# Kernel optimization log

Hardware: AMD Instinct MI355X
Metric: run time of the kernel (lower is better)

## Reference

```python
import jax, jax.numpy as jnp
import numpy as np

N_EDGES = 200_000
N_ANGLES = 1_000_000
D = 128          # atom_embed_dim
N_RBF = 6
A_DIM = 49       # n_spher * l_spher
N_BIL = 8        # n_bilinear


def _glorot(key, shape):
    fan_in, fan_out = shape[0], shape[-1]
    lim = jnp.sqrt(6.0 / (fan_in + fan_out))
    return jax.random.uniform(key, shape, jnp.float32, -lim, lim)


def setup_inputs() -> dict:
    key = jax.random.key(0)
    ks = jax.random.split(key, 10)
    m_ji = jax.random.normal(ks[0], (N_EDGES, D), jnp.float32)
    nbr_list = jax.random.randint(ks[1], (N_EDGES, 2), 0, 20000)
    angle_list = jax.random.randint(ks[2], (N_ANGLES, 3), 0, 20000)
    e_rbf = jax.random.normal(ks[3], (N_EDGES, N_RBF), jnp.float32)
    a_sbf = jax.random.normal(ks[4], (N_ANGLES, A_DIM), jnp.float32)
    kj_idx = jax.random.randint(ks[5], (N_ANGLES,), 0, N_EDGES)
    # parameters (torch Linear weight transposed to [in, out])
    W_nbr = _glorot(ks[6], (D, D))
    b_nbr = jnp.zeros((D,), jnp.float32)
    W_e = _glorot(ks[7], (N_RBF, D))
    W_a = _glorot(ks[8], (A_DIM, N_BIL))
    final_w = _glorot(ks[9], (D, N_BIL, D))  # [i, j, l]
    return {
        "m_ji": m_ji, "nbr_list": nbr_list, "angle_list": angle_list,
        "e_rbf": e_rbf, "a_sbf": a_sbf, "kj_idx": kj_idx,
        "W_nbr": W_nbr, "b_nbr": b_nbr, "W_e": W_e, "W_a": W_a,
        "final_w": final_w,
    }


def reference(m_ji, nbr_list, angle_list, e_rbf, a_sbf, kj_idx,
              W_nbr, b_nbr, W_e, W_a, final_w):
    # gather edge messages/radial features per angle (triplet)
    m_kj = m_ji[kj_idx]                                  # [W, D]
    transf_m = jax.nn.silu(m_kj @ W_nbr + b_nbr)         # swish(Linear)
    transf_e = e_rbf[kj_idx] @ W_e                       # [W, D]
    m_and_e = transf_m * transf_e                        # [W, D]
    transf_a = a_sbf @ W_a                               # [W, n_bilinear]
    # bilinear contraction per angle: out[w,i] = sum_{j,l} a[w,j] me[w,l] T[i,j,l]
    out = jnp.einsum('wj,wl,ijl->wi', transf_a, m_and_e, final_w)
    # scatter back to edges (dim_size = n_edges)
    final = jax.ops.segment_sum(out, kj_idx, num_segments=m_ji.shape[0])
    return final
```

## Files before the change

kernel.cpp:

```cpp
#include <hip/hip_runtime.h>
#include <math.h>

#define D 128
#define N_RBF 6
#define A_DIM 49
#define N_BIL 8
#define N_EDGES 200000
#define N_ANGLES 1000000

#define BM 128
#define THREADS 512
#define MROW 132

__device__ __forceinline__ int swz(int row, int col) {
  return (row << 7) + (col ^ (((row >> 3) & 7) << 2));
}

__global__ __launch_bounds__(256) void k_accA(const float* __restrict__ a_sbf,
                                              const int* __restrict__ kj,
                                              const float* __restrict__ W_a,
                                              float* __restrict__ A) {
  __shared__ float wa[A_DIM * N_BIL];
  for (int i = threadIdx.x; i < A_DIM * N_BIL; i += 256) wa[i] = W_a[i];
  __syncthreads();
  int w = blockIdx.x * 256 + threadIdx.x;
  const int stride = gridDim.x * 256;
  for (; w < N_ANGLES; w += stride) {
    const float* ar = a_sbf + (size_t)w * A_DIM;
    float ta[N_BIL];
#pragma unroll
    for (int j = 0; j < N_BIL; ++j) ta[j] = 0.f;
#pragma unroll
    for (int k = 0; k < A_DIM; ++k) {
      const float av = ar[k];
#pragma unroll
      for (int j = 0; j < N_BIL; ++j) ta[j] = fmaf(av, wa[k * N_BIL + j], ta[j]);
    }
    const int e = kj[w];
    float* Ae = A + (size_t)e * N_BIL;
#pragma unroll
    for (int j = 0; j < N_BIL; ++j) atomicAdd(Ae + j, ta[j]);
  }
}

__global__ __launch_bounds__(THREADS, 2) void k_main(const float* __restrict__ m_ji,
                                                     const float* __restrict__ e_rbf,
                                                     const float* __restrict__ W_nbr,
                                                     const float* __restrict__ b_nbr,
                                                     const float* __restrict__ W_e,
                                                     const float* __restrict__ T,
                                                     const float* __restrict__ A,
                                                     float* __restrict__ out) {
  __shared__ float me_lds[BM * MROW];
  __shared__ float tjb[D * D];
  __shared__ float A_lds[BM * N_BIL];
  __shared__ float we_lds[N_RBF * D];
  __shared__ float erbf_lds[BM * N_RBF];

  const int t = threadIdx.x;
  const int e0 = blockIdx.x * BM;
  const int tr = t >> 4;
  const int ti = t & 15;
  const int r0 = tr * 4;
  const int i0 = ti * 8;

  {
    const float4* gm = reinterpret_cast<const float4*>(m_ji);
#pragma unroll
    for (int it = 0; it < 8; ++it) {
      const int q = it * THREADS + t;
      const int r = q >> 5, c4 = q & 31;
      size_t grow = (size_t)(e0 + r);
      if (grow >= N_EDGES) grow = N_EDGES - 1;
      const float4 v = gm[grow * 32 + c4];
      *reinterpret_cast<float4*>(&me_lds[r * MROW + c4 * 4]) = v;
    }
  }
  {
    const float4* gw = reinterpret_cast<const float4*>(W_nbr);
#pragma unroll
    for (int it = 0; it < 8; ++it) {
      const int q = it * THREADS + t;
      const int k = q >> 5, i4 = q & 31;
      const float4 v = gw[k * 32 + i4];
      tjb[swz(i4 * 4 + 0, k)] = v.x;
      tjb[swz(i4 * 4 + 1, k)] = v.y;
      tjb[swz(i4 * 4 + 2, k)] = v.z;
      tjb[swz(i4 * 4 + 3, k)] = v.w;
    }
  }
  for (int q = t; q < BM * N_RBF; q += THREADS) {
    size_t g = (size_t)e0 * N_RBF + q;
    if (g >= (size_t)N_EDGES * N_RBF) g = (size_t)N_EDGES * N_RBF - 1;
    erbf_lds[q] = e_rbf[g];
  }
  for (int q = t; q < N_RBF * D; q += THREADS) we_lds[q] = W_e[q];
  for (int q = t; q < BM * N_BIL; q += THREADS) {
    size_t g = (size_t)e0 * N_BIL + q;
    if (g >= (size_t)N_EDGES * N_BIL) g = (size_t)N_EDGES * N_BIL - 1;
    A_lds[q] = A[g];
  }
  __syncthreads();

  float tm[4][8];
#pragma unroll
  for (int a = 0; a < 4; ++a)
#pragma unroll
    for (int b = 0; b < 8; ++b) tm[a][b] = 0.f;

#pragma unroll 2
  for (int kc = 0; kc < 32; ++kc) {
    float4 mv[4];
#pragma unroll
    for (int rr = 0; rr < 4; ++rr)
      mv[rr] = *reinterpret_cast<const float4*>(&me_lds[(r0 + rr) * MROW + kc * 4]);
    float4 wv[8];
#pragma unroll
    for (int ii = 0; ii < 8; ++ii)
      wv[ii] = *reinterpret_cast<const float4*>(&tjb[swz(i0 + ii, kc * 4)]);
#pragma unroll
    for (int rr = 0; rr < 4; ++rr)
#pragma unroll
      for (int ii = 0; ii < 8; ++ii) {
        tm[rr][ii] = fmaf(mv[rr].x, wv[ii].x, tm[rr][ii]);
        tm[rr][ii] = fmaf(mv[rr].y, wv[ii].y, tm[rr][ii]);
        tm[rr][ii] = fmaf(mv[rr].z, wv[ii].z, tm[rr][ii]);
        tm[rr][ii] = fmaf(mv[rr].w, wv[ii].w, tm[rr][ii]);
      }
  }

  float bi[8];
#pragma unroll
  for (int ii = 0; ii < 8; ++ii) bi[ii] = b_nbr[i0 + ii];
  float me[4][8];
#pragma unroll
  for (int rr = 0; rr < 4; ++rr)
#pragma unroll
    for (int ii = 0; ii < 8; ++ii) {
      const float x = tm[rr][ii] + bi[ii];
      const float s = x / (1.f + expf(-x));
      float te = 0.f;
#pragma unroll
      for (int q = 0; q < N_RBF; ++q)
        te = fmaf(erbf_lds[(r0 + rr) * N_RBF + q], we_lds[q * D + i0 + ii], te);
      me[rr][ii] = s * te;
    }
  __syncthreads();
#pragma unroll
  for (int rr = 0; rr < 4; ++rr)
#pragma unroll
    for (int ii = 0; ii < 8; ++ii) me_lds[(r0 + rr) * MROW + i0 + ii] = me[rr][ii];

  float acc[4][8];
#pragma unroll
  for (int a = 0; a < 4; ++a)
#pragma unroll
    for (int b = 0; b < 8; ++b) acc[a][b] = 0.f;

  for (int j = 0; j < N_BIL; ++j) {
    __syncthreads();
#pragma unroll
    for (int it = 0; it < 8; ++it) {
      const int q = it * THREADS + t;
      const int i = q >> 5, l4 = q & 31;
      const float4 v =
          *reinterpret_cast<const float4*>(&T[((size_t)i * N_BIL + j) * D + l4 * 4]);
      *reinterpret_cast<float4*>(&tjb[swz(i, l4 * 4)]) = v;
    }
    __syncthreads();

    float P[4][8];
#pragma unroll
    for (int a = 0; a < 4; ++a)
#pragma unroll
      for (int b = 0; b < 8; ++b) P[a][b] = 0.f;

#pragma unroll 2
    for (int lc = 0; lc < 32; ++lc) {
      float4 mev[4];
#pragma unroll
      for (int rr = 0; rr < 4; ++rr)
        mev[rr] = *reinterpret_cast<const float4*>(&me_lds[(r0 + rr) * MROW + lc * 4]);
      float4 tv[8];
#pragma unroll
      for (int ii = 0; ii < 8; ++ii)
        tv[ii] = *reinterpret_cast<const float4*>(&tjb[swz(i0 + ii, lc * 4)]);
#pragma unroll
      for (int rr = 0; rr < 4; ++rr)
#pragma unroll
        for (int ii = 0; ii < 8; ++ii) {
          P[rr][ii] = fmaf(mev[rr].x, tv[ii].x, P[rr][ii]);
          P[rr][ii] = fmaf(mev[rr].y, tv[ii].y, P[rr][ii]);
          P[rr][ii] = fmaf(mev[rr].z, tv[ii].z, P[rr][ii]);
          P[rr][ii] = fmaf(mev[rr].w, tv[ii].w, P[rr][ii]);
        }
    }
#pragma unroll
    for (int rr = 0; rr < 4; ++rr) {
      const float aj = A_lds[(r0 + rr) * N_BIL + j];
#pragma unroll
      for (int ii = 0; ii < 8; ++ii) acc[rr][ii] = fmaf(aj, P[rr][ii], acc[rr][ii]);
    }
  }

#pragma unroll
  for (int rr = 0; rr < 4; ++rr) {
    const int erow = e0 + r0 + rr;
    if (erow < N_EDGES) {
      float4 o0 = make_float4(acc[rr][0], acc[rr][1], acc[rr][2], acc[rr][3]);
      float4 o1 = make_float4(acc[rr][4], acc[rr][5], acc[rr][6], acc[rr][7]);
      float* op = out + (size_t)erow * D + i0;
      *reinterpret_cast<float4*>(op) = o0;
      *reinterpret_cast<float4*>(op + 4) = o1;
    }
  }
}

extern "C" void kernel_launch(void* const* d_in, const int* in_sizes, int n_in,
                              void* d_out, int out_size, void* d_ws, size_t ws_size,
                              hipStream_t stream) {
  const float* m_ji  = (const float*)d_in[0];
  const float* e_rbf = (const float*)d_in[3];
  const float* a_sbf = (const float*)d_in[4];
  const int*   kj    = (const int*)d_in[5];
  const float* W_nbr = (const float*)d_in[6];
  const float* b_nbr = (const float*)d_in[7];
  const float* W_e   = (const float*)d_in[8];
  const float* W_a   = (const float*)d_in[9];
  const float* T     = (const float*)d_in[10];

  float* A   = (float*)d_ws;
  float* out = (float*)d_out;

  hipMemsetAsync(A, 0, (size_t)N_EDGES * N_BIL * sizeof(float), stream);
  k_accA<<<(N_ANGLES + 255) / 256, 256, 0, stream>>>(a_sbf, kj, W_a, A);
  k_main<<<(N_EDGES + BM - 1) / BM, THREADS, 0, stream>>>(m_ji, e_rbf, W_nbr, b_nbr, W_e,
                                                          T, A, out);
}
```

Baseline: 1.636 ms.

## Stage a_sbf through LDS, prefetch T slices into registers, simplify swizzle addressing

k_accA now has each block stage its 256×49 slice of a_sbf into shared memory with coalesced float4 loads, replacing strided per-thread row reads, and drops the grid-stride loop. k_main prefetches the next T slice into registers while the current slice is consumed, precomputes the swizzle XOR offset per thread, raises inner-loop unrolling to 8, and removes the min-blocks launch bound. The larger LDS footprint in k_accA and the higher register pressure in k_main may reduce occupancy.

```diff
diff --git a/kernel.cpp b/kernel.cpp
--- a/kernel.cpp
+++ b/kernel.cpp
@@ -20,13 +20,33 @@
                                               const int* __restrict__ kj,
                                               const float* __restrict__ W_a,
                                               float* __restrict__ A) {
+  __shared__ float sa[256 * A_DIM];
   __shared__ float wa[A_DIM * N_BIL];
-  for (int i = threadIdx.x; i < A_DIM * N_BIL; i += 256) wa[i] = W_a[i];
+  const int t = threadIdx.x;
+  const int blk0 = blockIdx.x * 256;
+
+  for (int q = t; q < A_DIM * N_BIL; q += 256) wa[q] = W_a[q];
+  {
+    const size_t fbase = (size_t)blk0 * A_DIM;
+    const float4* g4 = reinterpret_cast<const float4*>(a_sbf + fbase);
+    const int remain4 = (int)(((size_t)N_ANGLES * A_DIM - fbase) >> 2);
+    float4* s4 = reinterpret_cast<float4*>(sa);
+#pragma unroll
+    for (int it = 0; it < (256 * A_DIM) / 4 / 256; ++it) {
+      const int q = it * 256 + t;
+      s4[q] = (q < remain4) ? g4[q] : make_float4(0.f, 0.f, 0.f, 0.f);
+    }
+    {
+      const int q = 12 * 256 + t;
+      if (q < (256 * A_DIM) / 4)
+        s4[q] = (q < remain4) ? g4[q] : make_float4(0.f, 0.f, 0.f, 0.f);
+    }
+  }
   __syncthreads();
-  int w = blockIdx.x * 256 + threadIdx.x;
-  const int stride = gridDim.x * 256;
-  for (; w < N_ANGLES; w += stride) {
-    const float* ar = a_sbf + (size_t)w * A_DIM;
+
+  const int w = blk0 + t;
+  if (w < N_ANGLES) {
+    const float* ar = &sa[t * A_DIM];
     float ta[N_BIL];
 #pragma unroll
     for (int j = 0; j < N_BIL; ++j) ta[j] = 0.f;
@@ -36,21 +56,20 @@
 #pragma unroll
       for (int j = 0; j < N_BIL; ++j) ta[j] = fmaf(av, wa[k * N_BIL + j], ta[j]);
     }
-    const int e = kj[w];
-    float* Ae = A + (size_t)e * N_BIL;
+    float* Ae = A + (size_t)kj[w] * N_BIL;
 #pragma unroll
     for (int j = 0; j < N_BIL; ++j) atomicAdd(Ae + j, ta[j]);
   }
 }
 
-__global__ __launch_bounds__(THREADS, 2) void k_main(const float* __restrict__ m_ji,
-                                                     const float* __restrict__ e_rbf,
-                                                     const float* __restrict__ W_nbr,
-                                                     const float* __restrict__ b_nbr,
-                                                     const float* __restrict__ W_e,
-                                                     const float* __restrict__ T,
-                                                     const float* __restrict__ A,
-                                                     float* __restrict__ out) {
+__global__ __launch_bounds__(THREADS) void k_main(const float* __restrict__ m_ji,
+                                                  const float* __restrict__ e_rbf,
+                                                  const float* __restrict__ W_nbr,
+                                                  const float* __restrict__ b_nbr,
+                                                  const float* __restrict__ W_e,
+                                                  const float* __restrict__ T,
+                                                  const float* __restrict__ A,
+                                                  float* __restrict__ out) {
   __shared__ float me_lds[BM * MROW];
   __shared__ float tjb[D * D];
   __shared__ float A_lds[BM * N_BIL];
@@ -63,6 +82,18 @@
   const int ti = t & 15;
   const int r0 = tr * 4;
   const int i0 = ti * 8;
+  const int cbx = (ti & 7) << 2;
+
+  const float* tvb = &tjb[i0 << 7];
+  const float* mvb = &me_lds[r0 * MROW];
+
+  float4 treg[8];
+#pragma unroll
+  for (int it = 0; it < 8; ++it) {
+    const int q = it * THREADS + t;
+    const int i = q >> 5, l4 = q & 31;
+    treg[it] = *reinterpret_cast<const float4*>(&T[((size_t)i * N_BIL + 0) * D + l4 * 4]);
+  }
 
   {
     const float4* gm = reinterpret_cast<const float4*>(m_ji);
@@ -108,16 +139,17 @@
 #pragma unroll
     for (int b = 0; b < 8; ++b) tm[a][b] = 0.f;
 
-#pragma unroll 2
+#pragma unroll 8
   for (int kc = 0; kc < 32; ++kc) {
+    const int so = (kc << 2) ^ cbx;
     float4 mv[4];
 #pragma unroll
     for (int rr = 0; rr < 4; ++rr)
-      mv[rr] = *reinterpret_cast<const float4*>(&me_lds[(r0 + rr) * MROW + kc * 4]);
+      mv[rr] = *reinterpret_cast<const float4*>(mvb + rr * MROW + (kc << 2));
     float4 wv[8];
 #pragma unroll
     for (int ii = 0; ii < 8; ++ii)
-      wv[ii] = *reinterpret_cast<const float4*>(&tjb[swz(i0 + ii, kc * 4)]);
+      wv[ii] = *reinterpret_cast<const float4*>(tvb + (ii << 7) + so);
 #pragma unroll
     for (int rr = 0; rr < 4; ++rr)
 #pragma unroll
@@ -163,9 +195,16 @@
     for (int it = 0; it < 8; ++it) {
       const int q = it * THREADS + t;
       const int i = q >> 5, l4 = q & 31;
-      const float4 v =
-          *reinterpret_cast<const float4*>(&T[((size_t)i * N_BIL + j) * D + l4 * 4]);
-      *reinterpret_cast<float4*>(&tjb[swz(i, l4 * 4)]) = v;
+      *reinterpret_cast<float4*>(&tjb[swz(i, l4 * 4)]) = treg[it];
+    }
+    if (j + 1 < N_BIL) {
+#pragma unroll
+      for (int it = 0; it < 8; ++it) {
+        const int q = it * THREADS + t;
+        const int i = q >> 5, l4 = q & 31;
+        treg[it] = *reinterpret_cast<const float4*>(
+            &T[((size_t)i * N_BIL + (j + 1)) * D + l4 * 4]);
+      }
     }
     __syncthreads();
 
@@ -175,16 +214,17 @@
 #pragma unroll
       for (int b = 0; b < 8; ++b) P[a][b] = 0.f;
 
-#pragma unroll 2
+#pragma unroll 8
     for (int lc = 0; lc < 32; ++lc) {
+      const int so = (lc << 2) ^ cbx;
       float4 mev[4];
 #pragma unroll
       for (int rr = 0; rr < 4; ++rr)
-        mev[rr] = *reinterpret_cast<const float4*>(&me_lds[(r0 + rr) * MROW + lc * 4]);
+        mev[rr] = *reinterpret_cast<const float4*>(mvb + rr * MROW + (lc << 2));
       float4 tv[8];
 #pragma unroll
       for (int ii = 0; ii < 8; ++ii)
-        tv[ii] = *reinterpret_cast<const float4*>(&tjb[swz(i0 + ii, lc * 4)]);
+        tv[ii] = *reinterpret_cast<const float4*>(tvb + (ii << 7) + so);
 #pragma unroll
       for (int rr = 0; rr < 4; ++rr)
 #pragma unroll
```

After: 1.892 ms. 15.6% more time.
